# Kernel optimization log

Hardware: AMD Instinct MI355X
Metric: run time of the kernel (lower is better)

## Reference

```python
import jax, jax.numpy as jnp
import numpy as np

N_WAY = 5
K_SHOT = 5
TEMPERATURE = 2.0
EPS = 1e-8


def setup_inputs() -> dict:
    key = jax.random.key(0)
    k1, k2, k3, k4 = jax.random.split(key, 4)
    b, q, c, h, w = 4, 75, 640, 10, 10
    support_xf = jax.random.normal(k1, (b, N_WAY * K_SHOT, c, h, w), jnp.float32)
    query_xf = jax.random.normal(k2, (b, q, c, h, w), jnp.float32)
    support_y = jax.random.randint(k3, (b, N_WAY * K_SHOT), 0, N_WAY)
    query_y = jax.random.randint(k4, (b, q), 0, N_WAY)
    return {"support_xf": support_xf, "support_y": support_y,
            "query_xf": query_xf, "query_y": query_y}


def reference(support_xf, support_y, query_xf, query_y):
    b, q, c, h, w = query_xf.shape
    M_q = h * w
    M_s = K_SHOT * h * w  # larger_shot == 'average' -> concat shot descriptors

    # support: [b, n_way*k_shot, c, h, w] -> [b, n_way, c, k_shot*h*w]
    sup = support_xf.reshape(b, N_WAY, K_SHOT, c, h * w)
    sup = jnp.transpose(sup, (0, 1, 3, 2, 4)).reshape(b, N_WAY, c, M_s)
    qf = query_xf.reshape(b, q, c, M_q)

    # cosine similarity over channel dim
    sn = sup / (jnp.linalg.norm(sup, axis=2, keepdims=True) + EPS)
    qn = qf / (jnp.linalg.norm(qf, axis=2, keepdims=True) + EPS)
    # S: [b, q, n_way, M_q, M_s]
    S = jnp.einsum('bqcm,bwcn->bqwmn', qn, sn)

    S_max = S.max(-1)  # [b, q, n_way, M_q]

    # nearest support descriptor (classes merged) for each query descriptor
    S_merged = jnp.transpose(S, (0, 1, 3, 2, 4)).reshape(b, q, M_q, N_WAY * M_s)
    query_nearest = jnp.argmax(S_merged, axis=-1)  # [b, q, M_q]

    # top-2 over class dim of per-class max similarity
    top2 = jax.lax.top_k(jnp.moveaxis(S_max, 2, -1), 2)[0]  # [b, q, M_q, 2]
    query_class_diff = top2[..., 0] - top2[..., 1]  # [b, q, M_q]

    # scatter diffs to the chosen support slot, take max over query positions
    diffs_m = jax.nn.one_hot(query_nearest, N_WAY * M_s, dtype=jnp.float32) \
        * query_class_diff[..., None]  # [b, q, M_q, n_way*M_s]
    diffs_max_nearest = jnp.argmax(diffs_m, axis=-2)  # [b, q, n_way*M_s]

    # mutual-nearest mask: query m is kept iff it is the best query for its slot
    sel = jnp.take_along_axis(diffs_max_nearest, query_nearest, axis=-1)  # [b,q,M_q]
    diff_mask = (sel == jnp.arange(M_q)).astype(jnp.float32) * TEMPERATURE

    predict = (S_max * diff_mask[:, :, None, :]).sum(-1).reshape(b * q, N_WAY)

    logp = jax.nn.log_softmax(predict, axis=-1)
    loss = -jnp.mean(jnp.take_along_axis(logp, query_y.reshape(-1, 1), axis=1))
    return loss
```

## Files before the change

kernel.cpp:

```cpp
#include <hip/hip_runtime.h>
#include <math.h>

#define BB 4
#define QQ 75
#define CC 640
#define HW 100
#define NWAY 5
#define KSHOT 5
#define MS 500
#define MSP 512
#define MTOT 7500
#define MPAD 7680
#define TEMPER 2.0f
#define EPSN 1e-8f
#define NCH 8
#define LBS 32768

typedef _Float16 v8h __attribute__((ext_vector_type(8)));
typedef float v4f __attribute__((ext_vector_type(4)));

__device__ inline void splitv(const float* x, v8h& hi, v8h& lo) {
#pragma unroll
    for (int j = 0; j < 8; ++j) {
        _Float16 h = (_Float16)x[j];
        float r0 = x[j] - (float)h;
        hi[j] = h; lo[j] = (_Float16)r0;
    }
}

typedef __attribute__((address_space(3))) unsigned int lds_uint;
typedef __attribute__((address_space(1))) const unsigned int glb_uint;
__device__ inline void gl_lds16(const void* g, void* l) {
    __builtin_amdgcn_global_load_lds((glb_uint*)g, (lds_uint*)l, 16, 0, 0);
}

__global__ __launch_bounds__(128) void norms(const float* __restrict__ qx,
                                             const float* __restrict__ sup,
                                             float* __restrict__ invq,
                                             float* __restrict__ invs,
                                             float* __restrict__ out) {
    int bid = blockIdx.x, t = threadIdx.x;
    if (bid == 0 && t == 0) out[0] = 0.f;
    const float* src; float* dst;
    if (bid < BB * QQ) { src = qx + (size_t)bid * CC * HW; dst = invq + bid * HW; }
    else { int bs = bid - BB * QQ; src = sup + (size_t)bs * CC * HW; dst = invs + bs * HW; }
    if (t < HW) {
        float ss = 0.f;
        for (int c = 0; c < CC; ++c) { float v = src[c * HW + t]; ss += v * v; }
        dst[t] = 1.f / (sqrtf(ss) + EPSN);
    }
}

__global__ __launch_bounds__(256) void prep_AB(const float* __restrict__ qx,
                                               const float* __restrict__ sup,
                                               const float* __restrict__ invs,
                                               _Float16* __restrict__ Ahi,
                                               _Float16* __restrict__ Alo,
                                               _Float16* __restrict__ Bhi,
                                               _Float16* __restrict__ Blo) {
    int g = blockIdx.x;
    const float* src; const float* inv = 0;
    _Float16 *dh, *dl;
    int ct;
    if (g < BB * QQ * 10) {
        int bq = g / 10; ct = g % 10;
        int b = bq / QQ, qi = bq % QQ;
        src = qx + ((size_t)bq * CC + ct * 64) * HW;
        size_t rowbase = (size_t)b * MPAD + qi * HW;
        dh = Ahi + rowbase * CC; dl = Alo + rowbase * CC;
    } else {
        int h = g - BB * QQ * 10;
        int bs = h / 10; ct = h % 10;
        int b = bs / 25, s = bs % 25, w = s / KSHOT, shot = s % KSHOT;
        src = sup + ((size_t)bs * CC + ct * 64) * HW;
        size_t rowbase = (size_t)(b * NWAY + w) * MSP + shot * HW;
        dh = Bhi + rowbase * CC; dl = Blo + rowbase * CC;
        inv = invs + bs * HW;
    }
    __shared__ float tile[64 * 101];
    __shared__ float invt[HW];
    int t = threadIdx.x;
    if (t < HW) invt[t] = inv ? inv[t] : 1.f;
    for (int i = t; i < 64 * HW; i += 256) tile[(i / HW) * 101 + (i % HW)] = src[i];
    __syncthreads();
    for (int cell = t; cell < 800; cell += 256) {
        int p = cell >> 3, oct = cell & 7;
        float iv = invt[p];
        float x[8];
#pragma unroll
        for (int j = 0; j < 8; ++j) x[j] = tile[(oct * 8 + j) * 101 + p] * iv;
        v8h hi, lo; splitv(x, hi, lo);
        size_t off = (size_t)p * CC + ct * 64 + oct * 8;
        *(v8h*)(dh + off) = hi;
        *(v8h*)(dl + off) = lo;
    }
}

__global__ __launch_bounds__(512, 2) void simkernel(
        const _Float16* __restrict__ Ahi, const _Float16* __restrict__ Alo,
        const _Float16* __restrict__ Bhi, const _Float16* __restrict__ Blo,
        float* __restrict__ pmax, unsigned short* __restrict__ pidx) {
    __shared__ char lds_raw[5 * LBS];

    int bid = blockIdx.x;
    int nt = bid % 10; int t2 = bid / 10;
    int mt = t2 % 30;  int b = t2 / 30;
    int m0 = mt * 256;
    int w = nt >> 1, n0w = (nt & 1) * 256;

    int tid = threadIdx.x;
    int lane = tid & 63;
    int wvu = __builtin_amdgcn_readfirstlane(tid >> 6);

    int arrA = wvu >> 2;
    int rgbase = (wvu & 3) * 4;
    const char* Ab = (const char*)((arrA ? Alo : Ahi) + ((size_t)b * MPAD + m0) * CC);
    const char* Bb = (const char*)((arrA ? Blo : Bhi) + ((size_t)(b * NWAY + w) * MSP + n0w) * CC);

    int rr0 = lane >> 2;
    int octsw = (lane & 3) ^ ((lane >> 3) & 3);
    int laneoff = rr0 * (CC * 2) + octsw * 16;

    const char* srcA[4]; const char* srcB[4]; int dof[4];
#pragma unroll
    for (int s = 0; s < 4; ++s) {
        int rg = rgbase + s;
        srcA[s] = Ab + (size_t)(rg * 16) * (CC * 2) + laneoff;
        srcB[s] = Bb + (size_t)(rg * 16) * (CC * 2) + laneoff;
        dof[s] = arrA * 16384 + rg * 1024;
    }
    char* ldsB = lds_raw + 2 * LBS;

    int wv = tid >> 6;
    int wm = wv >> 2, wn = wv & 3;
    int lq = lane >> 4, lc = lane & 15;

    int idxA[4], idxB[4];
#pragma unroll
    for (int mf = 0; mf < 4; ++mf) {
        int row = wm * 128 + mf * 16 + lc;
        idxA[mf] = row * 4 + (lq ^ ((row >> 1) & 3));
    }
#pragma unroll
    for (int nf = 0; nf < 4; ++nf) {
        int row = wn * 64 + nf * 16 + lc;
        idxB[nf] = row * 4 + (lq ^ ((row >> 1) & 3));
    }

    v4f acc[8][4];
#pragma unroll
    for (int mf = 0; mf < 8; ++mf)
#pragma unroll
        for (int nf = 0; nf < 4; ++nf) acc[mf][nf] = (v4f)0.f;

#pragma unroll
    for (int s = 0; s < 4; ++s) gl_lds16(srcA[s], lds_raw + dof[s]);
#pragma unroll
    for (int s = 0; s < 4; ++s) gl_lds16(srcB[s], ldsB + dof[s]);
#pragma unroll
    for (int s = 0; s < 4; ++s) gl_lds16(srcB[s] + 64, ldsB + LBS + dof[s]);
    asm volatile("s_waitcnt vmcnt(4)\n\ts_barrier" ::: "memory");

    for (int ch = 0; ch < 20; ++ch) {
        const char* cA = lds_raw + (ch & 1) * LBS;
        const char* cB = ldsB + (ch % 3) * LBS;
        const v8h* AHI = (const v8h*)cA;
        const v8h* ALO = (const v8h*)(cA + 16384);
        const v8h* BHI = (const v8h*)cB;
        const v8h* BLO = (const v8h*)(cB + 16384);
        char* nA = lds_raw + ((ch + 1) & 1) * LBS;
        char* nB = ldsB + ((ch + 2) % 3) * LBS;
        int offA = (ch + 1) * 64, offB = (ch + 2) * 64;

        v8h ahi[4], alo[4], a2hi[4], a2lo[4], bhi[4], blo[4];

#pragma unroll
        for (int m2 = 0; m2 < 4; ++m2) { ahi[m2] = AHI[idxA[m2]]; alo[m2] = ALO[idxA[m2]]; }
        bhi[0] = BHI[idxB[0]]; blo[0] = BLO[idxB[0]];
        bhi[1] = BHI[idxB[1]]; blo[1] = BLO[idxB[1]];
        if (ch < 19) {
#pragma unroll
            for (int s = 0; s < 4; ++s) gl_lds16(srcA[s] + offA, nA + dof[s]);
        }
        asm volatile("s_barrier\n\ts_waitcnt lgkmcnt(0)" ::: "memory");
        __builtin_amdgcn_s_setprio(1);
#pragma unroll
        for (int n2 = 0; n2 < 2; ++n2)
#pragma unroll
            for (int m2 = 0; m2 < 4; ++m2) {
                acc[m2][n2] = __builtin_amdgcn_mfma_f32_16x16x32_f16(ahi[m2], bhi[n2], acc[m2][n2], 0, 0, 0);
                acc[m2][n2] = __builtin_amdgcn_mfma_f32_16x16x32_f16(ahi[m2], blo[n2], acc[m2][n2], 0, 0, 0);
                acc[m2][n2] = __builtin_amdgcn_mfma_f32_16x16x32_f16(alo[m2], bhi[n2], acc[m2][n2], 0, 0, 0);
            }
        __builtin_amdgcn_s_setprio(0);

        bhi[2] = BHI[idxB[2]]; blo[2] = BLO[idxB[2]];
        bhi[3] = BHI[idxB[3]]; blo[3] = BLO[idxB[3]];
        if (ch < 18) { gl_lds16(srcB[0] + offB, nB + dof[0]); gl_lds16(srcB[1] + offB, nB + dof[1]); }
        asm volatile("s_barrier\n\ts_waitcnt lgkmcnt(0)" ::: "memory");
        __builtin_amdgcn_s_setprio(1);
#pragma unroll
        for (int n2 = 2; n2 < 4; ++n2)
#pragma unroll
            for (int m2 = 0; m2 < 4; ++m2) {
                acc[m2][n2] = __builtin_amdgcn_mfma_f32_16x16x32_f16(ahi[m2], bhi[n2], acc[m2][n2], 0, 0, 0);
                acc[m2][n2] = __builtin_amdgcn_mfma_f32_16x16x32_f16(ahi[m2], blo[n2], acc[m2][n2], 0, 0, 0);
                acc[m2][n2] = __builtin_amdgcn_mfma_f32_16x16x32_f16(alo[m2], bhi[n2], acc[m2][n2], 0, 0, 0);
            }
        __builtin_amdgcn_s_setprio(0);

#pragma unroll
        for (int m2 = 0; m2 < 4; ++m2) { a2hi[m2] = AHI[idxA[m2] + 256]; a2lo[m2] = ALO[idxA[m2] + 256]; }
        if (ch < 18) { gl_lds16(srcB[2] + offB, nB + dof[2]); gl_lds16(srcB[3] + offB, nB + dof[3]); }
        asm volatile("s_barrier\n\ts_waitcnt lgkmcnt(0)" ::: "memory");
        __builtin_amdgcn_s_setprio(1);
#pragma unroll
        for (int n2 = 0; n2 < 2; ++n2)
#pragma unroll
            for (int m2 = 0; m2 < 4; ++m2) {
                acc[4 + m2][n2] = __builtin_amdgcn_mfma_f32_16x16x32_f16(a2hi[m2], bhi[n2], acc[4 + m2][n2], 0, 0, 0);
                acc[4 + m2][n2] = __builtin_amdgcn_mfma_f32_16x16x32_f16(a2hi[m2], blo[n2], acc[4 + m2][n2], 0, 0, 0);
                acc[4 + m2][n2] = __builtin_amdgcn_mfma_f32_16x16x32_f16(a2lo[m2], bhi[n2], acc[4 + m2][n2], 0, 0, 0);
            }
        __builtin_amdgcn_s_setprio(0);

        if (ch < 18) asm volatile("s_waitcnt vmcnt(4)\n\ts_barrier" ::: "memory");
        else         asm volatile("s_waitcnt vmcnt(0)\n\ts_barrier" ::: "memory");
        __builtin_amdgcn_s_setprio(1);
#pragma unroll
        for (int n2 = 2; n2 < 4; ++n2)
#pragma unroll
            for (int m2 = 0; m2 < 4; ++m2) {
                acc[4 + m2][n2] = __builtin_amdgcn_mfma_f32_16x16x32_f16(a2hi[m2], bhi[n2], acc[4 + m2][n2], 0, 0, 0);
                acc[4 + m2][n2] = __builtin_amdgcn_mfma_f32_16x16x32_f16(a2hi[m2], blo[n2], acc[4 + m2][n2], 0, 0, 0);
                acc[4 + m2][n2] = __builtin_amdgcn_mfma_f32_16x16x32_f16(a2lo[m2], bhi[n2], acc[4 + m2][n2], 0, 0, 0);
            }
        __builtin_amdgcn_s_setprio(0);
    }

    int chunk = (nt & 1) * 4 + wn;
#pragma unroll
    for (int mf = 0; mf < 8; ++mf) {
#pragma unroll
        for (int r = 0; r < 4; ++r) {
            float v = -__builtin_inff(); int idx = 0x7fffffff;
#pragma unroll
            for (int nf = 0; nf < 4; ++nf) {
                int n_way = n0w + wn * 64 + nf * 16 + lc;
                float cv = acc[mf][nf][r];
                if (n_way < MS && cv > v) { v = cv; idx = n_way; }
            }
#pragma unroll
            for (int msk = 1; msk < 16; msk <<= 1) {
                float ov = __shfl_xor(v, msk);
                int oi = __shfl_xor(idx, msk);
                if (ov > v || (ov == v && oi < idx)) { v = ov; idx = oi; }
            }
            if (lc == 0) {
                int mrow = m0 + wm * 128 + mf * 16 + lq * 4 + r;
                size_t o = ((size_t)(b * NWAY + w) * NCH + chunk) * MPAD + mrow;
                pmax[o] = v;
                pidx[o] = (unsigned short)(idx & 0xffff);
            }
        }
    }
}

__global__ void norm_support(const float* __restrict__ sup, float* __restrict__ snre) {
    int bid = blockIdx.x;
    int b = bid / 25, s = bid % 25;
    int w = s / KSHOT, shot = s % KSHOT;
    const float* src = sup + (size_t)bid * CC * HW;
    float* dst = snre + ((size_t)(b * NWAY + w)) * CC * MSP + shot * HW;
    __shared__ float inv[HW];
    int t = threadIdx.x;
    if (t < HW) {
        float ss = 0.f;
        for (int c = 0; c < CC; ++c) { float v = src[c * HW + t]; ss += v * v; }
        inv[t] = 1.f / (sqrtf(ss) + EPSN);
    }
    __syncthreads();
    for (int i = t; i < CC * HW; i += 256) {
        int c = i / HW, p = i % HW;
        dst[c * MSP + p] = src[i] * inv[p];
    }
    if (shot == KSHOT - 1) {
        float* padbase = snre + ((size_t)(b * NWAY + w)) * CC * MSP;
        for (int i = t; i < CC * (MSP - MS); i += 256) {
            int c = i / (MSP - MS), j = i % (MSP - MS);
            padbase[c * MSP + MS + j] = 0.f;
        }
    }
}

__global__ __launch_bounds__(256) void simkernel_fb(
        const float* __restrict__ qx, const float* __restrict__ snre,
        float* __restrict__ pmax, unsigned short* __restrict__ pidx) {
    __shared__ char lds_fb[49152];
    v8h* AHI = (v8h*)(lds_fb);
    v8h* ALO = (v8h*)(lds_fb + 8192);
    v8h* BHI = (v8h*)(lds_fb + 16384);
    v8h* BLO = (v8h*)(lds_fb + 32768);

    int bid = blockIdx.x;
    int mt = bid % 60; int t2 = bid / 60;
    int nt = t2 % 10;  int b = t2 / 10;
    int m0 = mt * 128;
    int w = nt >> 1;
    int n0w = (nt & 1) * 256;

    int tid = threadIdx.x;
    const float* Abase = qx + (size_t)b * QQ * CC * HW;
    const float* Bbase = snre + (size_t)(b * NWAY + w) * CC * MSP;

    int oct = tid & 3;
    int arow = tid >> 2;
    int aqi[2], ap[2];
#pragma unroll
    for (int pass = 0; pass < 2; ++pass) {
        int mg = m0 + arow + pass * 64;
        if (mg >= MTOT) mg = 0;
        aqi[pass] = mg / HW; ap[pass] = mg % HW;
    }

    v4f acc[4][8];
#pragma unroll
    for (int mf = 0; mf < 4; ++mf)
#pragma unroll
        for (int nf = 0; nf < 8; ++nf) acc[mf][nf] = (v4f)0.f;

    int lane = tid & 63;
    int wv = tid >> 6;
    int mrow_w = (wv >> 1) * 64;
    int ncol_w = (wv & 1) * 128;
    int lq = lane >> 4, lc = lane & 15;

    for (int ch = 0; ch < 20; ++ch) {
        int c0 = ch * 32 + oct * 8;
        __syncthreads();
#pragma unroll
        for (int pass = 0; pass < 2; ++pass) {
            const float* src = Abase + ((size_t)aqi[pass] * CC + c0) * HW + ap[pass];
            float x[8];
#pragma unroll
            for (int j = 0; j < 8; ++j) x[j] = src[j * HW];
            v8h hi, lo; splitv(x, hi, lo);
            int cell = (arow + pass * 64) * 4 + oct;
            AHI[cell] = hi; ALO[cell] = lo;
        }
#pragma unroll
        for (int pass = 0; pass < 4; ++pass) {
            int nrow = arow + pass * 64;
            const float* src = Bbase + (size_t)c0 * MSP + n0w + nrow;
            float x[8];
#pragma unroll
            for (int j = 0; j < 8; ++j) x[j] = src[j * MSP];
            v8h hi, lo; splitv(x, hi, lo);
            int cell = nrow * 4 + oct;
            BHI[cell] = hi; BLO[cell] = lo;
        }
        __syncthreads();

        v8h ahi[4], alo[4];
#pragma unroll
        for (int mf = 0; mf < 4; ++mf) {
            int idx = (mrow_w + mf * 16 + lc) * 4 + lq;
            ahi[mf] = AHI[idx]; alo[mf] = ALO[idx];
        }
#pragma unroll
        for (int nf = 0; nf < 8; ++nf) {
            int idx = (ncol_w + nf * 16 + lc) * 4 + lq;
            v8h bhi = BHI[idx], blo = BLO[idx];
#pragma unroll
            for (int mf = 0; mf < 4; ++mf) {
                acc[mf][nf] = __builtin_amdgcn_mfma_f32_16x16x32_f16(ahi[mf], bhi, acc[mf][nf], 0, 0, 0);
                acc[mf][nf] = __builtin_amdgcn_mfma_f32_16x16x32_f16(ahi[mf], blo, acc[mf][nf], 0, 0, 0);
                acc[mf][nf] = __builtin_amdgcn_mfma_f32_16x16x32_f16(alo[mf], bhi, acc[mf][nf], 0, 0, 0);
            }
        }
    }

    int chunkidx = (nt & 1) * 2 + (wv & 1);
#pragma unroll
    for (int mf = 0; mf < 4; ++mf) {
#pragma unroll
        for (int r = 0; r < 4; ++r) {
            float v = -__builtin_inff(); int idx = 0x7fffffff;
#pragma unroll
            for (int nf = 0; nf < 8; ++nf) {
                int n_way = n0w + ncol_w + nf * 16 + lc;
                float cv = acc[mf][nf][r];
                if (n_way < MS && cv > v) { v = cv; idx = n_way; }
            }
#pragma unroll
            for (int msk = 1; msk < 16; msk <<= 1) {
                float ov = __shfl_xor(v, msk);
                int oi = __shfl_xor(idx, msk);
                if (ov > v || (ov == v && oi < idx)) { v = ov; idx = oi; }
            }
            if (lc == 0) {
                int mrow = m0 + mrow_w + mf * 16 + lq * 4 + r;
                size_t ob = (size_t)(b * NWAY + w) * NCH * MPAD + mrow;
                int s_hi = (idx != 0x7fffffff) ? (idx >> 6) : -1;
#pragma unroll
                for (int sl2 = 0; sl2 < 2; ++sl2) {
                    int sl = chunkidx * 2 + sl2;
                    if (sl == s_hi) {
                        pmax[ob + (size_t)sl * MPAD] = v;
                        pidx[ob + (size_t)sl * MPAD] = (unsigned short)(idx & 0xffff);
                    } else {
                        pmax[ob + (size_t)sl * MPAD] = -__builtin_inff();
                        pidx[ob + (size_t)sl * MPAD] = 0xffffu;
                    }
                }
            }
        }
    }
}

__global__ __launch_bounds__(128) void finalize(
        const float* __restrict__ pmax, const unsigned short* __restrict__ pidx,
        const float* __restrict__ invq, const int* __restrict__ qy,
        float* __restrict__ out) {
    int bq = blockIdx.x;
    int b = bq / QQ, qi = bq % QQ;
    __shared__ float sm[NWAY][HW];
    __shared__ int   si[NWAY][HW];
    __shared__ float diffv[HW];
    __shared__ int   nearest[HW];
    __shared__ float maskv[HW];
    __shared__ float pred[NWAY];
    int t = threadIdx.x;
    if (t < HW) {
        float iq = invq[bq * HW + t];
        for (int w = 0; w < NWAY; ++w) {
            size_t base = ((size_t)(b * NWAY + w) * NCH) * MPAD + qi * HW + t;
            float best = -__builtin_inff(); int bi = 0x7fffffff;
            for (int c = 0; c < NCH; ++c) {
                float v = pmax[base + (size_t)c * MPAD];
                if (v > best) { best = v; bi = pidx[base + (size_t)c * MPAD]; }
            }
            sm[w][t] = best * iq;
            si[w][t] = bi;
        }
    }
    __syncthreads();
    if (t < HW) {
        float v1 = -INFINITY, v2 = -INFINITY;
        float bestv = -INFINITY; int bestslot = 0;
        for (int w = 0; w < NWAY; ++w) {
            float v = sm[w][t];
            if (v > v1) { v2 = v1; v1 = v; } else if (v > v2) { v2 = v; }
            if (v > bestv) { bestv = v; bestslot = w * MS + si[w][t]; }
        }
        diffv[t] = v1 - v2;
        nearest[t] = bestslot;
    }
    __syncthreads();
    if (t < HW) {
        int slot = nearest[t];
        float bv = (nearest[0] == slot) ? diffv[0] : 0.f;
        int bm = 0;
        for (int m = 1; m < HW; ++m) {
            float val = (nearest[m] == slot) ? diffv[m] : 0.f;
            if (val > bv) { bv = val; bm = m; }
        }
        maskv[t] = (bm == t) ? TEMPER : 0.f;
    }
    __syncthreads();
    if (t < NWAY) {
        float s = 0.f;
        for (int m = 0; m < HW; ++m) s += sm[t][m] * maskv[m];
        pred[t] = s;
    }
    __syncthreads();
    if (t == 0) {
        float mx = pred[0];
        for (int w = 1; w < NWAY; ++w) mx = fmaxf(mx, pred[w]);
        float se = 0.f;
        for (int w = 0; w < NWAY; ++w) se += expf(pred[w] - mx);
        float lse = mx + logf(se);
        int y = qy[bq];
        atomicAdd(out, -(pred[y] - lse) * (1.f / (BB * QQ)));
    }
}

extern "C" void kernel_launch(void* const* d_in, const int* in_sizes, int n_in,
                              void* d_out, int out_size, void* d_ws, size_t ws_size,
                              hipStream_t stream) {
    const float* sup = (const float*)d_in[0];
    const float* qx  = (const float*)d_in[2];
    const int*   qy  = (const int*)d_in[3];
    float* out = (float*)d_out;

    size_t pcount = (size_t)BB * NWAY * NCH * MPAD;
    float* pmax = (float*)d_ws;
    unsigned short* pidx = (unsigned short*)(pmax + pcount);
    float* invq = (float*)(pidx + pcount);
    float* invs = invq + (size_t)BB * MTOT;
    char*  big = (char*)(invs + (size_t)BB * 25 * HW);
    size_t header = (size_t)(big - (char*)d_ws);
    size_t needA = (size_t)BB * MPAD * CC * 2;
    size_t needB = (size_t)BB * NWAY * MSP * CC * 2;
    size_t need_fast = header + 2 * (needA + needB);

    hipLaunchKernelGGL(norms, dim3(BB * QQ + BB * 25), dim3(128), 0, stream,
                       qx, sup, invq, invs, out);

    if (ws_size >= need_fast) {
        _Float16* Ahi = (_Float16*)big;
        _Float16* Alo = Ahi + (size_t)BB * MPAD * CC;
        _Float16* Bhi = Alo + (size_t)BB * MPAD * CC;
        _Float16* Blo = Bhi + (size_t)BB * NWAY * MSP * CC;
        hipLaunchKernelGGL(prep_AB, dim3(BB * QQ * 10 + BB * 25 * 10), dim3(256), 0, stream,
                           qx, sup, invs, Ahi, Alo, Bhi, Blo);
        hipLaunchKernelGGL(simkernel, dim3(BB * 30 * 10), dim3(512), 0, stream,
                           Ahi, Alo, Bhi, Blo, pmax, pidx);
    } else {
        float* snre = (float*)big;
        hipLaunchKernelGGL(norm_support, dim3(BB * 25), dim3(256), 0, stream, sup, snre);
        hipLaunchKernelGGL(simkernel_fb, dim3(BB * 10 * 60), dim3(256), 0, stream,
                           qx, snre, pmax, pidx);
    }
    hipLaunchKernelGGL(finalize, dim3(BB * QQ), dim3(128), 0, stream,
                       pmax, pidx, invq, qy, out);
}
```

Before: 464.9 us.

## Software-pipeline LDS fragment loads one MFMA phase ahead across chunks

Restructures the main GEMM loop so each LDS fragment read is issued one MFMA phase before it is consumed. The next chunk's A and B fragments are prefetched at the end of the current chunk, behind the vmcnt barrier. The explicit lgkmcnt(0) waits are dropped so the compiler can place the waits itself, letting LDS reads overlap the MFMA sequence. The risk is higher register pressure from live fragment registers, and correctness now depends on the barrier placement relative to the buffer being overwritten.

```diff
diff --git a/kernel.cpp b/kernel.cpp
--- a/kernel.cpp
+++ b/kernel.cpp
@@ -161,6 +161,18 @@
     for (int s = 0; s < 4; ++s) gl_lds16(srcB[s] + 64, ldsB + LBS + dof[s]);
     asm volatile("s_waitcnt vmcnt(4)\n\ts_barrier" ::: "memory");
 
+    v8h ahi[4], alo[4], a2hi[4], a2lo[4], bhi[4], blo[4];
+    {
+        const v8h* XAH = (const v8h*)lds_raw;
+        const v8h* XAL = (const v8h*)(lds_raw + 16384);
+        const v8h* XBH = (const v8h*)ldsB;
+        const v8h* XBL = (const v8h*)(ldsB + 16384);
+#pragma unroll
+        for (int m2 = 0; m2 < 4; ++m2) { ahi[m2] = XAH[idxA[m2]]; alo[m2] = XAL[idxA[m2]]; }
+        bhi[0] = XBH[idxB[0]]; blo[0] = XBL[idxB[0]];
+        bhi[1] = XBH[idxB[1]]; blo[1] = XBL[idxB[1]];
+    }
+
     for (int ch = 0; ch < 20; ++ch) {
         const char* cA = lds_raw + (ch & 1) * LBS;
         const char* cB = ldsB + (ch % 3) * LBS;
@@ -170,19 +182,17 @@
         const v8h* BLO = (const v8h*)(cB + 16384);
         char* nA = lds_raw + ((ch + 1) & 1) * LBS;
         char* nB = ldsB + ((ch + 2) % 3) * LBS;
+        const char* xA = lds_raw + ((ch + 1) & 1) * LBS;
+        const char* xB = ldsB + ((ch + 1) % 3) * LBS;
         int offA = (ch + 1) * 64, offB = (ch + 2) * 64;
 
-        v8h ahi[4], alo[4], a2hi[4], a2lo[4], bhi[4], blo[4];
-
-#pragma unroll
-        for (int m2 = 0; m2 < 4; ++m2) { ahi[m2] = AHI[idxA[m2]]; alo[m2] = ALO[idxA[m2]]; }
-        bhi[0] = BHI[idxB[0]]; blo[0] = BLO[idxB[0]];
-        bhi[1] = BHI[idxB[1]]; blo[1] = BLO[idxB[1]];
+        asm volatile("s_barrier" ::: "memory");
         if (ch < 19) {
 #pragma unroll
             for (int s = 0; s < 4; ++s) gl_lds16(srcA[s] + offA, nA + dof[s]);
         }
-        asm volatile("s_barrier\n\ts_waitcnt lgkmcnt(0)" ::: "memory");
+        bhi[2] = BHI[idxB[2]]; blo[2] = BLO[idxB[2]];
+        bhi[3] = BHI[idxB[3]]; blo[3] = BLO[idxB[3]];
         __builtin_amdgcn_s_setprio(1);
 #pragma unroll
         for (int n2 = 0; n2 < 2; ++n2)
@@ -194,10 +204,10 @@
             }
         __builtin_amdgcn_s_setprio(0);
 
-        bhi[2] = BHI[idxB[2]]; blo[2] = BLO[idxB[2]];
-        bhi[3] = BHI[idxB[3]]; blo[3] = BLO[idxB[3]];
+        asm volatile("s_barrier" ::: "memory");
         if (ch < 18) { gl_lds16(srcB[0] + offB, nB + dof[0]); gl_lds16(srcB[1] + offB, nB + dof[1]); }
-        asm volatile("s_barrier\n\ts_waitcnt lgkmcnt(0)" ::: "memory");
+#pragma unroll
+        for (int m2 = 0; m2 < 4; ++m2) { a2hi[m2] = AHI[idxA[m2] + 256]; a2lo[m2] = ALO[idxA[m2] + 256]; }
         __builtin_amdgcn_s_setprio(1);
 #pragma unroll
         for (int n2 = 2; n2 < 4; ++n2)
@@ -209,10 +219,8 @@
             }
         __builtin_amdgcn_s_setprio(0);
 
-#pragma unroll
-        for (int m2 = 0; m2 < 4; ++m2) { a2hi[m2] = AHI[idxA[m2] + 256]; a2lo[m2] = ALO[idxA[m2] + 256]; }
+        asm volatile("s_barrier" ::: "memory");
         if (ch < 18) { gl_lds16(srcB[2] + offB, nB + dof[2]); gl_lds16(srcB[3] + offB, nB + dof[3]); }
-        asm volatile("s_barrier\n\ts_waitcnt lgkmcnt(0)" ::: "memory");
         __builtin_amdgcn_s_setprio(1);
 #pragma unroll
         for (int n2 = 0; n2 < 2; ++n2)
@@ -226,6 +234,17 @@
 
         if (ch < 18) asm volatile("s_waitcnt vmcnt(4)\n\ts_barrier" ::: "memory");
         else         asm volatile("s_waitcnt vmcnt(0)\n\ts_barrier" ::: "memory");
+
+        if (ch < 19) {
+            const v8h* XAH = (const v8h*)xA;
+            const v8h* XAL = (const v8h*)(xA + 16384);
+            const v8h* XBH = (const v8h*)xB;
+            const v8h* XBL = (const v8h*)(xB + 16384);
+#pragma unroll
+            for (int m2 = 0; m2 < 4; ++m2) { ahi[m2] = XAH[idxA[m2]]; alo[m2] = XAL[idxA[m2]]; }
+            bhi[0] = XBH[idxB[0]]; blo[0] = XBL[idxB[0]];
+            bhi[1] = XBH[idxB[1]]; blo[1] = XBL[idxB[1]];
+        }
         __builtin_amdgcn_s_setprio(1);
 #pragma unroll
         for (int n2 = 2; n2 < 4; ++n2)
```

New measurement: 481.0 us. 3.5% more time.

## Software-pipeline LDS fragment reads across MFMA phases with inline ds_read

Applied to the files above, without the earlier changes.

Replaces compiler-generated LDS loads with inline ds_read_b128 pairs that use immediate offsets. The reads are issued one phase ahead, including a prefetch of the next chunk's A and B fragments before the final MFMA block. Barriers are split from the waitcnts, which now use partial lgkmcnt counts, and sched_barriers pin the ordering so LDS latency overlaps with MFMA execution. This adds register pressure and relies on hand-counted waitcnt values being correct.

```diff
diff --git a/kernel.cpp b/kernel.cpp
--- a/kernel.cpp
+++ b/kernel.cpp
@@ -30,9 +30,20 @@
 
 typedef __attribute__((address_space(3))) unsigned int lds_uint;
 typedef __attribute__((address_space(1))) const unsigned int glb_uint;
+typedef __attribute__((address_space(3))) const v8h* lds_v8hp;
 __device__ inline void gl_lds16(const void* g, void* l) {
     __builtin_amdgcn_global_load_lds((glb_uint*)g, (lds_uint*)l, 16, 0, 0);
 }
+
+#define DSR2(h_, l_, p_, I0, I1) \
+    asm volatile("ds_read_b128 %0, %2 offset:" I0 "\n\t" \
+                 "ds_read_b128 %1, %2 offset:" I1 \
+                 : "=v"(h_), "=v"(l_) : "v"((lds_v8hp)(p_)))
+
+#define MFMA3(ACC, AH, AL, BH, BL) \
+    ACC = __builtin_amdgcn_mfma_f32_16x16x32_f16(AH, BH, ACC, 0, 0, 0); \
+    ACC = __builtin_amdgcn_mfma_f32_16x16x32_f16(AH, BL, ACC, 0, 0, 0); \
+    ACC = __builtin_amdgcn_mfma_f32_16x16x32_f16(AL, BH, ACC, 0, 0, 0);
 
 __global__ __launch_bounds__(128) void norms(const float* __restrict__ qx,
                                              const float* __restrict__ sup,
@@ -135,16 +146,16 @@
     int wm = wv >> 2, wn = wv & 3;
     int lq = lane >> 4, lc = lane & 15;
 
-    int idxA[4], idxB[4];
+    int aA[4], aB[4];
 #pragma unroll
     for (int mf = 0; mf < 4; ++mf) {
         int row = wm * 128 + mf * 16 + lc;
-        idxA[mf] = row * 4 + (lq ^ ((row >> 1) & 3));
+        aA[mf] = (row * 4 + (lq ^ ((row >> 1) & 3))) * 16;
     }
 #pragma unroll
     for (int nf = 0; nf < 4; ++nf) {
         int row = wn * 64 + nf * 16 + lc;
-        idxB[nf] = row * 4 + (lq ^ ((row >> 1) & 3));
+        aB[nf] = (row * 4 + (lq ^ ((row >> 1) & 3))) * 16;
     }
 
     v4f acc[8][4];
@@ -160,81 +171,76 @@
 #pragma unroll
     for (int s = 0; s < 4; ++s) gl_lds16(srcB[s] + 64, ldsB + LBS + dof[s]);
     asm volatile("s_waitcnt vmcnt(4)\n\ts_barrier" ::: "memory");
+
+    v8h ahi[4], alo[4], a2hi[4], a2lo[4], bhi[4], blo[4];
+#pragma unroll
+    for (int m2 = 0; m2 < 4; ++m2) { DSR2(ahi[m2], alo[m2], lds_raw + aA[m2], "0", "16384"); }
+    DSR2(bhi[0], blo[0], ldsB + aB[0], "0", "16384");
+    DSR2(bhi[1], blo[1], ldsB + aB[1], "0", "16384");
 
     for (int ch = 0; ch < 20; ++ch) {
         const char* cA = lds_raw + (ch & 1) * LBS;
         const char* cB = ldsB + (ch % 3) * LBS;
-        const v8h* AHI = (const v8h*)cA;
-        const v8h* ALO = (const v8h*)(cA + 16384);
-        const v8h* BHI = (const v8h*)cB;
-        const v8h* BLO = (const v8h*)(cB + 16384);
         char* nA = lds_raw + ((ch + 1) & 1) * LBS;
         char* nB = ldsB + ((ch + 2) % 3) * LBS;
+        const char* xA = nA;
+        const char* xB = ldsB + ((ch + 1) % 3) * LBS;
         int offA = (ch + 1) * 64, offB = (ch + 2) * 64;
 
-        v8h ahi[4], alo[4], a2hi[4], a2lo[4], bhi[4], blo[4];
-
-#pragma unroll
-        for (int m2 = 0; m2 < 4; ++m2) { ahi[m2] = AHI[idxA[m2]]; alo[m2] = ALO[idxA[m2]]; }
-        bhi[0] = BHI[idxB[0]]; blo[0] = BLO[idxB[0]];
-        bhi[1] = BHI[idxB[1]]; blo[1] = BLO[idxB[1]];
+        asm volatile("s_barrier" ::: "memory");
         if (ch < 19) {
 #pragma unroll
             for (int s = 0; s < 4; ++s) gl_lds16(srcA[s] + offA, nA + dof[s]);
         }
-        asm volatile("s_barrier\n\ts_waitcnt lgkmcnt(0)" ::: "memory");
+        DSR2(bhi[2], blo[2], cB + aB[2], "0", "16384");
+        DSR2(bhi[3], blo[3], cB + aB[3], "0", "16384");
+        asm volatile("s_waitcnt lgkmcnt(4)" ::: "memory");
+        __builtin_amdgcn_sched_barrier(0);
         __builtin_amdgcn_s_setprio(1);
 #pragma unroll
         for (int n2 = 0; n2 < 2; ++n2)
 #pragma unroll
-            for (int m2 = 0; m2 < 4; ++m2) {
-                acc[m2][n2] = __builtin_amdgcn_mfma_f32_16x16x32_f16(ahi[m2], bhi[n2], acc[m2][n2], 0, 0, 0);
-                acc[m2][n2] = __builtin_amdgcn_mfma_f32_16x16x32_f16(ahi[m2], blo[n2], acc[m2][n2], 0, 0, 0);
-                acc[m2][n2] = __builtin_amdgcn_mfma_f32_16x16x32_f16(alo[m2], bhi[n2], acc[m2][n2], 0, 0, 0);
-            }
+            for (int m2 = 0; m2 < 4; ++m2) { MFMA3(acc[m2][n2], ahi[m2], alo[m2], bhi[n2], blo[n2]); }
         __builtin_amdgcn_s_setprio(0);
 
-        bhi[2] = BHI[idxB[2]]; blo[2] = BLO[idxB[2]];
-        bhi[3] = BHI[idxB[3]]; blo[3] = BLO[idxB[3]];
+        asm volatile("s_barrier" ::: "memory");
         if (ch < 18) { gl_lds16(srcB[0] + offB, nB + dof[0]); gl_lds16(srcB[1] + offB, nB + dof[1]); }
-        asm volatile("s_barrier\n\ts_waitcnt lgkmcnt(0)" ::: "memory");
+#pragma unroll
+        for (int m2 = 0; m2 < 4; ++m2) { DSR2(a2hi[m2], a2lo[m2], cA + aA[m2], "4096", "20480"); }
+        asm volatile("s_waitcnt lgkmcnt(8)" ::: "memory");
+        __builtin_amdgcn_sched_barrier(0);
         __builtin_amdgcn_s_setprio(1);
 #pragma unroll
         for (int n2 = 2; n2 < 4; ++n2)
 #pragma unroll
-            for (int m2 = 0; m2 < 4; ++m2) {
-                acc[m2][n2] = __builtin_amdgcn_mfma_f32_16x16x32_f16(ahi[m2], bhi[n2], acc[m2][n2], 0, 0, 0);
-                acc[m2][n2] = __builtin_amdgcn_mfma_f32_16x16x32_f16(ahi[m2], blo[n2], acc[m2][n2], 0, 0, 0);
-                acc[m2][n2] = __builtin_amdgcn_mfma_f32_16x16x32_f16(alo[m2], bhi[n2], acc[m2][n2], 0, 0, 0);
-            }
+            for (int m2 = 0; m2 < 4; ++m2) { MFMA3(acc[m2][n2], ahi[m2], alo[m2], bhi[n2], blo[n2]); }
         __builtin_amdgcn_s_setprio(0);
 
-#pragma unroll
-        for (int m2 = 0; m2 < 4; ++m2) { a2hi[m2] = AHI[idxA[m2] + 256]; a2lo[m2] = ALO[idxA[m2] + 256]; }
+        asm volatile("s_barrier" ::: "memory");
         if (ch < 18) { gl_lds16(srcB[2] + offB, nB + dof[2]); gl_lds16(srcB[3] + offB, nB + dof[3]); }
-        asm volatile("s_barrier\n\ts_waitcnt lgkmcnt(0)" ::: "memory");
+        asm volatile("s_waitcnt lgkmcnt(0)" ::: "memory");
+        __builtin_amdgcn_sched_barrier(0);
         __builtin_amdgcn_s_setprio(1);
 #pragma unroll
         for (int n2 = 0; n2 < 2; ++n2)
 #pragma unroll
-            for (int m2 = 0; m2 < 4; ++m2) {
-                acc[4 + m2][n2] = __builtin_amdgcn_mfma_f32_16x16x32_f16(a2hi[m2], bhi[n2], acc[4 + m2][n2], 0, 0, 0);
-                acc[4 + m2][n2] = __builtin_amdgcn_mfma_f32_16x16x32_f16(a2hi[m2], blo[n2], acc[4 + m2][n2], 0, 0, 0);
-                acc[4 + m2][n2] = __builtin_amdgcn_mfma_f32_16x16x32_f16(a2lo[m2], bhi[n2], acc[4 + m2][n2], 0, 0, 0);
-            }
+            for (int m2 = 0; m2 < 4; ++m2) { MFMA3(acc[4 + m2][n2], a2hi[m2], a2lo[m2], bhi[n2], blo[n2]); }
         __builtin_amdgcn_s_setprio(0);
 
         if (ch < 18) asm volatile("s_waitcnt vmcnt(4)\n\ts_barrier" ::: "memory");
         else         asm volatile("s_waitcnt vmcnt(0)\n\ts_barrier" ::: "memory");
+
+        if (ch < 19) {
+#pragma unroll
+            for (int m2 = 0; m2 < 4; ++m2) { DSR2(ahi[m2], alo[m2], xA + aA[m2], "0", "16384"); }
+            DSR2(bhi[0], blo[0], xB + aB[0], "0", "16384");
+            DSR2(bhi[1], blo[1], xB + aB[1], "0", "16384");
+        }
         __builtin_amdgcn_s_setprio(1);
 #pragma unroll
         for (int n2 = 2; n2 < 4; ++n2)
 #pragma unroll
-            for (int m2 = 0; m2 < 4; ++m2) {
-                acc[4 + m2][n2] = __builtin_amdgcn_mfma_f32_16x16x32_f16(a2hi[m2], bhi[n2], acc[4 + m2][n2], 0, 0, 0);
-                acc[4 + m2][n2] = __builtin_amdgcn_mfma_f32_16x16x32_f16(a2hi[m2], blo[n2], acc[4 + m2][n2], 0, 0, 0);
-                acc[4 + m2][n2] = __builtin_amdgcn_mfma_f32_16x16x32_f16(a2lo[m2], bhi[n2], acc[4 + m2][n2], 0, 0, 0);
-            }
+            for (int m2 = 0; m2 < 4; ++m2) { MFMA3(acc[4 + m2][n2], a2hi[m2], a2lo[m2], bhi[n2], blo[n2]); }
         __builtin_amdgcn_s_setprio(0);
     }
 
```

Result: slower. 475.6 us (+2.3%).
